# Optimization experiments

Measured on AMD Instinct MI355X. Metric: run time of the kernel, lower is better.

## Reference

```python
import jax, jax.numpy as jnp
import numpy as np

WEIGHT = 1000.0      # start/end cell penalty
LONELY_W = 15.0      # cell lit outside cluster
CLUSTER_W = 5.0      # cell unlit inside cluster
CELL_W = 20.0        # cell on a shortest manhattan path
CSIZE_W = 12.0       # cluster-size penalty
GAP_W = 300.0        # gap-to-endpoint penalty
H = W = 10


def _md(y1, x1, y2, x2):
    return jnp.abs(y1 - y2) + jnp.abs(x1 - x2)


def _per_sample(result, points):
    # result: [H, W] float, points: [2, 2] int (row, col) of start and end
    p0y, p0x = points[0, 0], points[0, 1]
    p1y, p1x = points[1, 0], points[1, 1]
    base = _md(p0y, p0x, p1y, p1x)

    loss_start = (2.0 - (result[p0y, p0x] + result[p1y, p1x])) * WEIGHT

    # 8-connected flood fill from start over cells whose value rounds to 1.
    mask = jnp.round(result) == 1.0
    seed = jnp.zeros((H, W), bool).at[p0y, p0x].set(True)

    def dilate(_, c):
        p = jnp.pad(c, 1)
        nb = (p[:-2, :-2] | p[:-2, 1:-1] | p[:-2, 2:] |
              p[1:-1, :-2] | p[1:-1, 2:] |
              p[2:, :-2] | p[2:, 1:-1] | p[2:, 2:])
        return c | (nb & mask)

    # 8-connected diameter of a 10x10 grid is 9; H+W iterations is a safe bound.
    cluster = jax.lax.fori_loop(0, H + W, dilate, seed)

    rows = jnp.arange(H)[:, None]
    cols = jnp.arange(W)[None, :]

    # per-cell manhattan detour penalty
    d2 = _md(rows, cols, p0y, p0x) + _md(rows, cols, p1y, p1x)
    delta = (d2 - base).astype(result.dtype)
    single_cell = jnp.sum(jnp.where(delta == 0.0,
                                    (1.0 - result) * CELL_W,
                                    result * delta * 0.5))

    # NB: the original tests [column, row] membership against [row, col]
    # cluster entries -> transposed membership map. Faithfully reproduced.
    in_cl = cluster.T
    csize = jnp.sum(cluster).astype(result.dtype)
    lonelyness = jnp.sum(jnp.where(in_cl, (1.0 - result) * CLUSTER_W,
                                   result * LONELY_W))
    cluster_size_pen = jnp.sum(jnp.where(in_cl, result * csize * CSIZE_W, 0.0))

    # nearest cluster cell to the end point (strict improvement over base)
    dist_end = _md(rows, cols, p1y, p1x)
    masked = jnp.where(cluster, dist_end, H * W + 10).reshape(-1)
    idx = jnp.argmin(masked)
    minval = masked[idx]
    better = minval < base
    ny = jnp.where(better, idx // W, p0y)
    nx = jnp.where(better, idx % W, p0x)
    gap = jnp.minimum(base, minval)

    oy = p1y - ny
    ox = p1x - nx

    def upd(cond, cy, cx, st):
        by, bx, bg = st
        d = _md(cy, cx, p1y, p1x)
        b = cond & (d < bg)
        return (jnp.where(b, cy, by), jnp.where(b, cx, bx), jnp.where(b, d, bg))

    st = (ny, nx, gap)
    c = ox < 0
    st = upd(c, ny, nx - 1, st)
    st = upd(c & (ny != 0), ny - 1, nx - 1, st)
    st = upd(c & (ny != H - 1), ny + 1, nx - 1, st)
    c = ox > 0
    st = upd(c, ny, nx + 1, st)
    st = upd(c & (ny != 0), ny - 1, nx + 1, st)
    st = upd(c & (ny != H - 1), ny + 1, nx + 1, st)
    st = upd(oy < 0, ny - 1, nx, st)
    st = upd(oy > 0, ny + 1, nx, st)
    ncy = jnp.clip(st[0], 0, H - 1)
    ncx = jnp.clip(st[1], 0, W - 1)

    gap_pen = gap.astype(result.dtype) * GAP_W * (1.0 - result[ncy, ncx])

    return loss_start + lonelyness + single_cell + cluster_size_pen + gap_pen


def setup_inputs() -> dict:
    key = jax.random.key(0)
    k1, k2 = jax.random.split(key)
    B = 262144
    result_given = jax.random.uniform(k1, (B, 1, H, W), dtype=jnp.float32)
    points_given = jax.random.randint(k2, (B, 2, 2), 0, 10, dtype=jnp.int64 if jax.config.jax_enable_x64 else jnp.int32)
    return {"result_given": result_given, "points_given": points_given}


def reference(result_given, points_given):
    losses = jax.vmap(_per_sample)(result_given[:, 0], points_given)
    return jnp.sum(losses).reshape(1)
```

## Files before the change

### kernel.cpp

```cpp
#include <hip/hip_runtime.h>
#include <cstdint>

#define GH 10
#define GW 10

__global__ __launch_bounds__(256, 1) void custom_loss_kernel(
    const float* __restrict__ result,
    const int* __restrict__ points,
    float* __restrict__ out,
    int B)
{
    const int t = blockIdx.x * blockDim.x + threadIdx.x;
    float loss = 0.f;
    if (t < B) {
        const float* __restrict__ r = result + (size_t)t * 100;
        const int4 p = ((const int4*)points)[t];
        const int p0y = p.x, p0x = p.y, p1y = p.z, p1x = p.w;
        const int base = abs(p0y - p1y) + abs(p0x - p1x);
        const int idx0 = p0y * GW + p0x;
        const int idx1 = p1y * GW + p1x;

        int ady[GH], adx[GW];
#pragma unroll
        for (int i = 0; i < GH; ++i) {
            ady[i] = abs(i - p0y) + abs(i - p1y) - abs(p0y - p1y);
            adx[i] = abs(i - p0x) + abs(i - p1x) - abs(p0x - p1x);
        }

        float rv[100];
        uint64_t mlo = 0, mhi = 0;
        float sum_all = 0.f, single_cell = 0.f, rs = 0.f, re = 0.f;
#pragma unroll
        for (int i = 0; i < 25; ++i) {
            const float4 v = ((const float4*)r)[i];
            const float vv[4] = {v.x, v.y, v.z, v.w};
#pragma unroll
            for (int k = 0; k < 4; ++k) {
                const int j = i * 4 + k;
                const float x = vv[k];
                rv[j] = x;
                sum_all += x;
                if (j == idx0) rs = x;
                if (j == idx1) re = x;
                const uint64_t bit = (x > 0.5f) ? 1ull : 0ull;
                if (j < 50) mlo |= bit << j; else mhi |= bit << (j - 50);
                const int delta = ady[j / 10] + adx[j % 10];
                single_cell += (delta == 0) ? (1.f - x) * 20.f
                                            : x * (float)delta * 0.5f;
            }
        }

        const uint64_t M50 = (1ull << 50) - 1;
        const uint64_t C0  = 0x10040100401ull;
        const uint64_t NC0 = M50 & ~C0;
        const uint64_t NC9 = M50 & ~(C0 << 9);
        uint64_t clo = 0, chi = 0;
        if (idx0 < 50) clo = 1ull << idx0; else chi = 1ull << (idx0 - 50);
#pragma unroll 1
        for (int it = 0; it < GH + GW; ++it) {
            const uint64_t hlo = clo | ((clo << 1) & NC0) | ((clo >> 1) & NC9);
            const uint64_t hhi = chi | ((chi << 1) & NC0) | ((chi >> 1) & NC9);
            uint64_t nlo = (hlo | (hlo << 10) | (hlo >> 10) | ((hhi & 0x3FFull) << 40)) & mlo;
            uint64_t nhi = (hhi | (hhi << 10) | (hhi >> 10) | (hlo >> 40)) & mhi;
            nlo |= clo; nhi |= chi;
            if (nlo == clo && nhi == chi) break;
            clo = nlo; chi = nhi;
        }

        const int K = __popcll(clo) + __popcll(chi);

        int bestd = 1000, bidx = 0;
#pragma unroll
        for (int y = 0; y < GH; ++y) {
            const uint32_t rb = (uint32_t)((y < 5 ? (clo >> (10 * y))
                                                  : (chi >> (10 * (y - 5)))) & 0x3FFull);
            const uint32_t left  = rb & ((2u << p1x) - 1);
            const uint32_t right = rb >> p1x;
            const int dl = left  ? (p1x - (31 - __builtin_clz(left))) : 1000;
            const int dr = right ? __builtin_ctz(right) : 1000;
            int dx, xx;
            if (dl <= dr) { dx = dl; xx = p1x - dl; }
            else          { dx = dr; xx = p1x + dr; }
            const int d = abs(y - p1y) + dx;
            if (rb && d < bestd) { bestd = d; bidx = y * GW + xx; }
        }

        const bool better = bestd < base;
        const int ny = better ? bidx / 10 : p0y;
        const int nx = better ? bidx % 10 : p0x;
        const int gap = min(base, bestd);

        int by = ny, bx = nx, bg = gap;
        const int oy = p1y - ny, ox = p1x - nx;
        auto upd = [&](bool cond, int cy, int cx) {
            const int d = abs(cy - p1y) + abs(cx - p1x);
            if (cond && (d < bg)) { by = cy; bx = cx; bg = d; }
        };
        upd(ox < 0,                    ny,     nx - 1);
        upd((ox < 0) && (ny != 0),     ny - 1, nx - 1);
        upd((ox < 0) && (ny != GH - 1),ny + 1, nx - 1);
        upd(ox > 0,                    ny,     nx + 1);
        upd((ox > 0) && (ny != 0),     ny - 1, nx + 1);
        upd((ox > 0) && (ny != GH - 1),ny + 1, nx + 1);
        upd(oy < 0,                    ny - 1, nx);
        upd(oy > 0,                    ny + 1, nx);
        const int ncy = min(max(by, 0), GH - 1);
        const int ncx = min(max(bx, 0), GW - 1);
        const int flatn = ncy * GW + ncx;

        float S_T = 0.f, rn = 0.f;
#pragma unroll
        for (int b = 0; b < 100; ++b) {
            const bool bit = (((b < 50 ? (clo >> b) : (chi >> (b - 50)))) & 1ull) != 0;
            const int tj = (b % 10) * 10 + (b / 10);
            const float x = rv[tj];
            if (bit) S_T += x;
            if (tj == flatn) rn = x;
        }

        const float csf = (float)K;
        const float loss_start = (2.f - (rs + re)) * 1000.f;
        const float lon  = 5.f * csf + 15.f * sum_all - 20.f * S_T;
        const float cpen = 12.f * csf * S_T;
        const float gap_pen = (float)gap * 300.f * (1.f - rn);
        loss = loss_start + lon + single_cell + cpen + gap_pen;
    }

#pragma unroll
    for (int off = 32; off > 0; off >>= 1)
        loss += __shfl_down(loss, off);
    __shared__ float wsum[4];
    const int lane = threadIdx.x & 63;
    const int wid = threadIdx.x >> 6;
    if (lane == 0) wsum[wid] = loss;
    __syncthreads();
    if (threadIdx.x == 0)
        atomicAdd(out, wsum[0] + wsum[1] + wsum[2] + wsum[3]);
}

extern "C" void kernel_launch(void* const* d_in, const int* in_sizes, int n_in,
                              void* d_out, int out_size, void* d_ws, size_t ws_size,
                              hipStream_t stream)
{
    const float* result = (const float*)d_in[0];
    const int* points   = (const int*)d_in[1];
    float* out = (float*)d_out;
    const int B = in_sizes[0] / 100;
    hipMemsetAsync(out, 0, sizeof(float), stream);
    const int block = 256;
    const int grid = (B + block - 1) / block;
    custom_loss_kernel<<<grid, block, 0, stream>>>(result, points, out, B);
}
```

Baseline: 202.8 us.

## Restructure per-sample loss to cut registers and raise occupancy

Splits the 100-cell tile into two 50-float halves and reloads the first half after the flood fill instead of keeping all 100 values live, with launch bounds raised to 4 waves per SIMD. The single-cell term is rewritten algebraically as separable row/column FMA sums plus an in-box correction, and the start, end and neighbour values are read directly from global memory rather than selected by compare chains. It also drops the per-element conditional selects in the transposed cluster sum. The intent is lower VGPR pressure and fewer ALU ops per sample, at the cost of redundant global/L2 loads.

After: 247.3 us. +22.0%, slower.

```diff
diff --git a/kernel.cpp b/kernel.cpp
--- a/kernel.cpp
+++ b/kernel.cpp
@@ -4,7 +4,67 @@
 #define GH 10
 #define GW 10
 
-__global__ __launch_bounds__(256, 1) void custom_loss_kernel(
+__device__ __forceinline__ void load5(const float* __restrict__ rp, float* v) {
+#pragma unroll
+    for (int i = 0; i < 5; ++i) {
+        const float4 a = *(const float4*)(rp + i * 10);
+        const float4 b = *(const float4*)(rp + i * 10 + 4);
+        const float2 c = *(const float2*)(rp + i * 10 + 8);
+        v[i*10+0]=a.x; v[i*10+1]=a.y; v[i*10+2]=a.z; v[i*10+3]=a.w;
+        v[i*10+4]=b.x; v[i*10+5]=b.y; v[i*10+6]=b.z; v[i*10+7]=b.w;
+        v[i*10+8]=c.x; v[i*10+9]=c.y;
+    }
+}
+
+template<int Y0>
+__device__ __forceinline__ void pass1_chunk(const float* v, int p0y, int p1y, int dy0,
+                                            const float* adxf, const float* inboxf,
+                                            float& sum_all, float& sc, float& boxSum,
+                                            uint64_t& mword)
+{
+#pragma unroll
+    for (int i = 0; i < 5; ++i) {
+        const int y = Y0 + i;
+        const float* vv = v + i * 10;
+        const float rowacc = ((vv[0]+vv[1])+(vv[2]+vv[3])) +
+                             ((vv[4]+vv[5])+(vv[6]+vv[7])) + (vv[8]+vv[9]);
+        sum_all += rowacc;
+        const int ay = abs(y - p0y) + abs(y - p1y) - dy0;
+        sc = fmaf((float)ay, rowacc, sc);
+        float boxrow = 0.f;
+        uint32_t rm = 0u;
+#pragma unroll
+        for (int x = 0; x < 10; ++x) {
+            const float xv = vv[x];
+            sc = fmaf(adxf[x], xv, sc);
+            boxrow = fmaf(inboxf[x], xv, boxrow);
+            rm |= (xv > 0.5f) ? (1u << x) : 0u;
+        }
+        boxSum += (ay == 0) ? boxrow : 0.f;
+        mword |= (uint64_t)rm << (10 * i);
+    }
+}
+
+template<int Y0>
+__device__ __forceinline__ float pass2_chunk(const float* v, uint64_t clo, uint64_t chi)
+{
+    float s = 0.f;
+#pragma unroll
+    for (int i = 0; i < 5; ++i) {
+        const int y = Y0 + i;
+        const float* vv = v + i * 10;
+#pragma unroll
+        for (int x = 0; x < 10; ++x) {
+            const int b = x * 10 + y;
+            const uint32_t bit = (b < 50) ? (uint32_t)((clo >> b) & 1ull)
+                                          : (uint32_t)((chi >> (b - 50)) & 1ull);
+            s = fmaf((float)bit, vv[x], s);
+        }
+    }
+    return s;
+}
+
+__global__ __launch_bounds__(256, 4) void custom_loss_kernel(
     const float* __restrict__ result,
     const int* __restrict__ points,
     float* __restrict__ out,
@@ -16,44 +76,33 @@
         const float* __restrict__ r = result + (size_t)t * 100;
         const int4 p = ((const int4*)points)[t];
         const int p0y = p.x, p0x = p.y, p1y = p.z, p1x = p.w;
-        const int base = abs(p0y - p1y) + abs(p0x - p1x);
-        const int idx0 = p0y * GW + p0x;
-        const int idx1 = p1y * GW + p1x;
+        const int dy0 = abs(p0y - p1y), dx0 = abs(p0x - p1x);
+        const int base = dy0 + dx0;
+        const float rs = r[p0y * GW + p0x];
+        const float re = r[p1y * GW + p1x];
 
-        int ady[GH], adx[GW];
+        float adxf[10], inboxf[10];
 #pragma unroll
-        for (int i = 0; i < GH; ++i) {
-            ady[i] = abs(i - p0y) + abs(i - p1y) - abs(p0y - p1y);
-            adx[i] = abs(i - p0x) + abs(i - p1x) - abs(p0x - p1x);
+        for (int x = 0; x < 10; ++x) {
+            const int a = abs(x - p0x) + abs(x - p1x) - dx0;
+            adxf[x] = (float)a;
+            inboxf[x] = (a == 0) ? 1.f : 0.f;
         }
 
-        float rv[100];
+        float sum_all = 0.f, sc = 0.f, boxSum = 0.f;
         uint64_t mlo = 0, mhi = 0;
-        float sum_all = 0.f, single_cell = 0.f, rs = 0.f, re = 0.f;
-#pragma unroll
-        for (int i = 0; i < 25; ++i) {
-            const float4 v = ((const float4*)r)[i];
-            const float vv[4] = {v.x, v.y, v.z, v.w};
-#pragma unroll
-            for (int k = 0; k < 4; ++k) {
-                const int j = i * 4 + k;
-                const float x = vv[k];
-                rv[j] = x;
-                sum_all += x;
-                if (j == idx0) rs = x;
-                if (j == idx1) re = x;
-                const uint64_t bit = (x > 0.5f) ? 1ull : 0ull;
-                if (j < 50) mlo |= bit << j; else mhi |= bit << (j - 50);
-                const int delta = ady[j / 10] + adx[j % 10];
-                single_cell += (delta == 0) ? (1.f - x) * 20.f
-                                            : x * (float)delta * 0.5f;
-            }
-        }
+
+        float vA[50], vB[50];
+        load5(r, vA);
+        pass1_chunk<0>(vA, p0y, p1y, dy0, adxf, inboxf, sum_all, sc, boxSum, mlo);
+        load5(r + 50, vB);
+        pass1_chunk<5>(vB, p0y, p1y, dy0, adxf, inboxf, sum_all, sc, boxSum, mhi);
 
         const uint64_t M50 = (1ull << 50) - 1;
         const uint64_t C0  = 0x10040100401ull;
         const uint64_t NC0 = M50 & ~C0;
         const uint64_t NC9 = M50 & ~(C0 << 9);
+        const int idx0 = p0y * GW + p0x;
         uint64_t clo = 0, chi = 0;
         if (idx0 < 50) clo = 1ull << idx0; else chi = 1ull << (idx0 - 50);
 #pragma unroll 1
@@ -68,6 +117,8 @@
         }
 
         const int K = __popcll(clo) + __popcll(chi);
+
+        load5(r, vA);
 
         int bestd = 1000, bidx = 0;
 #pragma unroll
@@ -96,31 +147,25 @@
             const int d = abs(cy - p1y) + abs(cx - p1x);
             if (cond && (d < bg)) { by = cy; bx = cx; bg = d; }
         };
-        upd(ox < 0,                    ny,     nx - 1);
-        upd((ox < 0) && (ny != 0),     ny - 1, nx - 1);
-        upd((ox < 0) && (ny != GH - 1),ny + 1, nx - 1);
-        upd(ox > 0,                    ny,     nx + 1);
-        upd((ox > 0) && (ny != 0),     ny - 1, nx + 1);
-        upd((ox > 0) && (ny != GH - 1),ny + 1, nx + 1);
-        upd(oy < 0,                    ny - 1, nx);
-        upd(oy > 0,                    ny + 1, nx);
+        upd(ox < 0,                     ny,     nx - 1);
+        upd((ox < 0) && (ny != 0),      ny - 1, nx - 1);
+        upd((ox < 0) && (ny != GH - 1), ny + 1, nx - 1);
+        upd(ox > 0,                     ny,     nx + 1);
+        upd((ox > 0) && (ny != 0),      ny - 1, nx + 1);
+        upd((ox > 0) && (ny != GH - 1), ny + 1, nx + 1);
+        upd(oy < 0,                     ny - 1, nx);
+        upd(oy > 0,                     ny + 1, nx);
         const int ncy = min(max(by, 0), GH - 1);
         const int ncx = min(max(bx, 0), GW - 1);
-        const int flatn = ncy * GW + ncx;
+        const float rn = r[ncy * GW + ncx];
 
-        float S_T = 0.f, rn = 0.f;
-#pragma unroll
-        for (int b = 0; b < 100; ++b) {
-            const bool bit = (((b < 50 ? (clo >> b) : (chi >> (b - 50)))) & 1ull) != 0;
-            const int tj = (b % 10) * 10 + (b / 10);
-            const float x = rv[tj];
-            if (bit) S_T += x;
-            if (tj == flatn) rn = x;
-        }
+        const float S_T = pass2_chunk<0>(vA, clo, chi) + pass2_chunk<5>(vB, clo, chi);
 
         const float csf = (float)K;
+        const float nboxf = (float)((dy0 + 1) * (dx0 + 1));
         const float loss_start = (2.f - (rs + re)) * 1000.f;
-        const float lon  = 5.f * csf + 15.f * sum_all - 20.f * S_T;
+        const float lon = 5.f * csf + 15.f * sum_all - 20.f * S_T;
+        const float single_cell = 0.5f * sc + 20.f * (nboxf - boxSum);
         const float cpen = 12.f * csf * S_T;
         const float gap_pen = (float)gap * 300.f * (1.f - rn);
         loss = loss_start + lon + single_cell + cpen + gap_pen;
```
